# Optimization experiments

Hardware: AMD Instinct MI355X
Metric: run time of the kernel (lower is better)

## Reference

```python
import jax, jax.numpy as jnp
import numpy as np

EPS = 1e-5
NEG_SLOPE = 0.2

def _conv1x1(x, w):
    # x: (B,C,N,K), w: (O,C) -> (B,O,N,K)
    return jnp.einsum('oc,bcnk->bonk', w, x)

def _bn(x, g, b, m, v):
    scale = g / jnp.sqrt(v + EPS)
    return x * scale[None, :, None, None] + (b - m * scale)[None, :, None, None]

def _lrelu(x):
    return jnp.where(x > 0, x, NEG_SLOPE * x)

def setup_inputs() -> dict:
    key = jax.random.key(0)
    specs = {
        'x': ((8, 6, 8192, 20), 'randn'),
        'trans_w': ((64, 6), 'randn'), 'trans_g': ((64,), 'rand'), 'trans_b': ((64,), 'randn'),
        'trans_m': ((64,), 'randn'), 'trans_v': ((64,), 'rand'),
        'pos_w1': ((64, 3), 'randn'), 'pos_g': ((64,), 'rand'), 'pos_b': ((64,), 'randn'),
        'pos_m': ((64,), 'randn'), 'pos_v': ((64,), 'rand'),
        'pos_w2': ((64, 64), 'randn'), 'pos_b2': ((64,), 'randn'),
        'gate_w1': ((16, 6), 'randn'), 'gate_g': ((16,), 'rand'), 'gate_b': ((16,), 'randn'),
        'gate_m': ((16,), 'randn'), 'gate_v': ((16,), 'rand'),
        'gate_w2': ((1, 16), 'randn'), 'gate_b2': ((1,), 'ones'),
        'attn_w1': ((16, 6), 'randn'), 'attn_g': ((16,), 'rand'), 'attn_b': ((16,), 'randn'),
        'attn_m': ((16,), 'randn'), 'attn_v': ((16,), 'rand'),
        'attn_w2': ((64, 16), 'randn'), 'attn_b2': ((64,), 'randn'),
    }
    out = {}
    for i, (name, (shape, fill)) in enumerate(specs.items()):
        k = jax.random.fold_in(key, i)
        if fill == 'randn':
            out[name] = jax.random.normal(k, shape, dtype=jnp.float32) * 0.1
        elif fill == 'rand':
            out[name] = jax.random.uniform(k, shape, dtype=jnp.float32)
        else:  # ones (gate bias init to 2.0 in original; scale ones)
            out[name] = jnp.ones(shape, dtype=jnp.float32) * 2.0
    return out

def reference(x, trans_w, trans_g, trans_b, trans_m, trans_v,
              pos_w1, pos_g, pos_b, pos_m, pos_v, pos_w2, pos_b2,
              gate_w1, gate_g, gate_b, gate_m, gate_v, gate_w2, gate_b2,
              attn_w1, attn_g, attn_b, attn_m, attn_v, attn_w2, attn_b2):
    in_channels = 3
    rel_pos = x[:, in_channels:in_channels + 3, :, :]  # (B,3,N,K)
    # pos_net: conv(3->C) + BN + LReLU + conv(C->C, bias)
    pos_h = _lrelu(_bn(_conv1x1(rel_pos, pos_w1), pos_g, pos_b, pos_m, pos_v))
    pos_enc = _conv1x1(pos_h, pos_w2) + pos_b2[None, :, None, None]
    # trans: conv(2*Cin->C) + BN + LReLU
    trans_feat = _lrelu(_bn(_conv1x1(x, trans_w), trans_g, trans_b, trans_m, trans_v)) + pos_enc
    # gate_net: conv(6->16)+BN+LReLU+conv(16->1,bias)+sigmoid (dropout=0 in eval)
    gate_h = _lrelu(_bn(_conv1x1(x, gate_w1), gate_g, gate_b, gate_m, gate_v))
    gate_map = jax.nn.sigmoid(_conv1x1(gate_h, gate_w2) + gate_b2[None, :, None, None])  # (B,1,N,K)
    clean_feat = trans_feat * gate_map
    # attn_net: conv(6->16)+BN+LReLU+conv(16->C,bias), then + pos_enc, softmax over K
    attn_h = _lrelu(_bn(_conv1x1(x, attn_w1), attn_g, attn_b, attn_m, attn_v))
    attn_logits = _conv1x1(attn_h, attn_w2) + attn_b2[None, :, None, None] + pos_enc
    attn_weights = jax.nn.softmax(attn_logits, axis=-1)
    out_attn = (trans_feat * attn_weights).sum(axis=-1)  # (B,C,N)
    out_max = clean_feat.max(axis=-1)                    # (B,C,N)
    return out_attn + out_max
```

## Files before the change

kernel.cpp:

```cpp
#include <hip/hip_runtime.h>
#include <math.h>

#define NEG 0.2f
#define EPSV 1e-5f

typedef _Float16 v8h __attribute__((ext_vector_type(8)));
typedef _Float16 v4h __attribute__((ext_vector_type(4)));
typedef _Float16 v2h __attribute__((ext_vector_type(2)));
typedef __fp16   f16x2 __attribute__((ext_vector_type(2)));
typedef float    v4f __attribute__((ext_vector_type(4)));

__device__ __forceinline__ float lrelu(float v) { return fmaxf(v, NEG * v); }
__device__ __forceinline__ v4f lrelu4(v4f v) {
    return __builtin_elementwise_max(v, v * NEG);
}
__device__ __forceinline__ v2h lreluh2(v2h v) {
    return __builtin_elementwise_max(v, v * (_Float16)NEG);
}

__device__ __forceinline__ v2h pk(float a, float b) {
    union { f16x2 i; v2h o; } u;
    u.i = __builtin_amdgcn_cvt_pkrtz(a, b);
    return u.o;
}

#define MFMA(a, b, c) __builtin_amdgcn_mfma_f32_16x16x32_f16((a), (b), (c), 0, 0, 0)

__global__ __launch_bounds__(256, 1)
void gsl_mfma(const float* __restrict__ x,
              const float* __restrict__ trans_w, const float* __restrict__ trans_g,
              const float* __restrict__ trans_b, const float* __restrict__ trans_m,
              const float* __restrict__ trans_v,
              const float* __restrict__ pos_w1, const float* __restrict__ pos_g,
              const float* __restrict__ pos_b, const float* __restrict__ pos_m,
              const float* __restrict__ pos_v, const float* __restrict__ pos_w2,
              const float* __restrict__ pos_b2,
              const float* __restrict__ gate_w1, const float* __restrict__ gate_g,
              const float* __restrict__ gate_b, const float* __restrict__ gate_m,
              const float* __restrict__ gate_v, const float* __restrict__ gate_w2,
              const float* __restrict__ gate_b2,
              const float* __restrict__ attn_w1, const float* __restrict__ attn_g,
              const float* __restrict__ attn_b, const float* __restrict__ attn_m,
              const float* __restrict__ attn_v, const float* __restrict__ attn_w2,
              const float* __restrict__ attn_b2,
              float* __restrict__ out)
{
    __shared__ _Float16 WH[3840];
    __shared__ float    PB2[64];
    __shared__ _Float16 PHB[4][2][1152];
    __shared__ _Float16 AHB[4][2][448];

    const int tid  = threadIdx.x;
    const int wv   = tid >> 6;
    const int lane = tid & 63;
    const int p    = lane & 15;
    const int q    = lane >> 4;

    const int b = blockIdx.x >> 7;
    const int n = ((blockIdx.x & 127) << 6) | (wv << 4) | p;

    {
        _Float16* AH0 = &AHB[wv][0][0];
        const v4h zh = {(_Float16)0.f, (_Float16)0.f, (_Float16)0.f, (_Float16)0.f};
        for (int i = lane; i < 224; i += 64) *(v4h*)(AH0 + 4 * i) = zh;
    }

    if (tid < 64) {
        const int c = tid;
        float sp = pos_g[c] * rsqrtf(pos_v[c] + EPSV);
        float bp = pos_b[c] - pos_m[c] * sp;
        _Float16* row = WH + (c >> 4) * 640 + (c & 15) * 40;
        for (int k = 0; k < 40; ++k) {
            float v = (k >= 3 && k < 6) ? pos_w1[c * 3 + (k - 3)] * sp
                                        : ((k == 6) ? bp : 0.f);
            row[k] = (_Float16)v;
        }
        PB2[c] = pos_b2[c];
    } else if (tid < 80) {
        const int j = tid - 64;
        float sa = attn_g[j] * rsqrtf(attn_v[j] + EPSV);
        float ba = attn_b[j] - attn_m[j] * sa;
        _Float16* row = WH + 2560 + j * 40;
        for (int k = 0; k < 40; ++k)
            row[k] = (_Float16)((k < 6) ? attn_w1[j * 6 + k] * sa
                                        : ((k == 6) ? ba : 0.f));
    } else if (tid < 96) {
        const int j = tid - 80;
        float sg = gate_g[j] * rsqrtf(gate_v[j] + EPSV);
        float bg = gate_b[j] - gate_m[j] * sg;
        _Float16* row = WH + 3200 + j * 40;
        for (int k = 0; k < 40; ++k)
            row[k] = (_Float16)((k < 6) ? gate_w1[j * 6 + k] * sg
                                        : ((k == 6) ? bg : 0.f));
    }

    v8h W2f[4][2], WTf[4], WA2f[4];
    #pragma unroll
    for (int mt = 0; mt < 4; ++mt) {
        const int ch = mt * 16 + p;
        #pragma unroll
        for (int h = 0; h < 2; ++h)
            #pragma unroll
            for (int i = 0; i < 8; ++i)
                W2f[mt][h][i] = (_Float16)pos_w2[ch * 64 + h * 32 + q * 8 + i];
        #pragma unroll
        for (int i = 0; i < 8; ++i) {
            int k = q * 8 + i;
            WA2f[mt][i] = (k < 16) ? (_Float16)attn_w2[ch * 16 + k] : (_Float16)0.f;
        }
        float st = trans_g[ch] * rsqrtf(trans_v[ch] + EPSV);
        float bt = trans_b[ch] - trans_m[ch] * st;
        #pragma unroll
        for (int i = 0; i < 8; ++i) {
            int k = q * 8 + i;
            float v = (k < 6) ? trans_w[ch * 6 + k] * st : ((k == 6) ? bt : 0.f);
            WTf[mt][i] = (_Float16)v;
        }
    }
    float g2w[4];
    #pragma unroll
    for (int r = 0; r < 4; ++r) g2w[r] = gate_w2[4 * q + r];
    const float gb2v = gate_b2[0];

    __syncthreads();

    const _Float16* const WP1p = WH + p * 40 + q * 8;
    const _Float16* const WA1p = WH + 2560 + p * 40 + q * 8;
    const _Float16* const WG1p = WH + 3200 + p * 40 + q * 8;
    const float* const    PB2p = PB2 + 4 * q;

    _Float16* const PHbase = &PHB[wv][0][0];
    _Float16* const AHbase = &AHB[wv][0][0];

    const v4f zero = {0.f, 0.f, 0.f, 0.f};
    v4f den[4], num[4], cmx[4];
    #pragma unroll
    for (int mt = 0; mt < 4; ++mt) {
        den[mt] = zero; num[mt] = zero;
        cmx[mt] = (v4f){-3.4e38f, -3.4e38f, -3.4e38f, -3.4e38f};
    }

    const float* xb = x + ((size_t)(b * 6) * 8192 + n) * 20;

    float nx[6];
    #pragma unroll
    for (int c = 0; c < 6; ++c) nx[c] = xb[(size_t)c * 163840];

    v8h xv_cur;
    {
        union { v8h v; v2h h[4]; } u;
        u.h[0] = pk(nx[0], nx[1]);
        u.h[1] = pk(nx[2], nx[3]);
        u.h[2] = pk(nx[4], nx[5]);
        u.h[3] = (v2h){(_Float16)1.f, (_Float16)0.f};
        xv_cur = u.v;
    }
    #pragma unroll
    for (int c = 0; c < 6; ++c) nx[c] = xb[(size_t)c * 163840 + 1];

    {
        v4f php[4];
        #pragma unroll
        for (int mt = 0; mt < 4; ++mt)
            php[mt] = MFMA(*(const v8h*)(WP1p + mt * 640), xv_cur, zero);
        v4f ahp = MFMA(*(const v8h*)WA1p, xv_cur, zero);
        _Float16* PHW = PHbase + p * 72 + 4 * q;
        #pragma unroll
        for (int mt = 0; mt < 4; ++mt) {
            union { v4h v; v2h h[2]; } u;
            u.h[0] = lreluh2(pk(php[mt][0], php[mt][1]));
            u.h[1] = lreluh2(pk(php[mt][2], php[mt][3]));
            *(v4h*)(PHW + mt * 16) = u.v;
        }
        union { v4h v; v2h h[2]; } ua;
        ua.h[0] = lreluh2(pk(ahp[0], ahp[1]));
        ua.h[1] = lreluh2(pk(ahp[2], ahp[3]));
        *(v4h*)(AHbase + p * 24 + 4 * q) = ua.v;
    }

    #pragma unroll 1
    for (int k = 0; k < 20; ++k) {
        const int sel = k & 1;
        _Float16* PH = PHbase + sel * 1152;
        _Float16* AH = AHbase + sel * 448;
        v8h phf0 = *(const v8h*)(PH + p * 72 + 8 * q);
        v8h phf1 = *(const v8h*)(PH + p * 72 + 32 + 8 * q);
        v8h ahf  = *(const v8h*)(AH + p * 24 + 8 * q);

        v8h xv_nxt = xv_cur;
        if (k < 19) {
            union { v8h v; v2h h[4]; } u;
            u.h[0] = pk(nx[0], nx[1]);
            u.h[1] = pk(nx[2], nx[3]);
            u.h[2] = pk(nx[4], nx[5]);
            u.h[3] = (v2h){(_Float16)1.f, (_Float16)0.f};
            xv_nxt = u.v;
            const int kn = (k < 18) ? k + 2 : 19;
            #pragma unroll
            for (int c = 0; c < 6; ++c) nx[c] = xb[(size_t)c * 163840 + kn];

            v4f php[4];
            #pragma unroll
            for (int mt = 0; mt < 4; ++mt)
                php[mt] = MFMA(*(const v8h*)(WP1p + mt * 640), xv_nxt, zero);
            v4f ahp = MFMA(*(const v8h*)WA1p, xv_nxt, zero);
            _Float16* PHW = PHbase + (sel ^ 1) * 1152 + p * 72 + 4 * q;
            #pragma unroll
            for (int mt = 0; mt < 4; ++mt) {
                union { v4h v; v2h h[2]; } uu;
                uu.h[0] = lreluh2(pk(php[mt][0], php[mt][1]));
                uu.h[1] = lreluh2(pk(php[mt][2], php[mt][3]));
                *(v4h*)(PHW + mt * 16) = uu.v;
            }
            union { v4h v; v2h h[2]; } ua;
            ua.h[0] = lreluh2(pk(ahp[0], ahp[1]));
            ua.h[1] = lreluh2(pk(ahp[2], ahp[3]));
            *(v4h*)(AHbase + (sel ^ 1) * 448 + p * 24 + 4 * q) = ua.v;
        }

        v4f tfa[4];
        #pragma unroll
        for (int mt = 0; mt < 4; ++mt) tfa[mt] = MFMA(WTf[mt], xv_cur, zero);
        v4f ghp = MFMA(*(const v8h*)WG1p, xv_cur, zero);
        float ga = 0.f;
        #pragma unroll
        for (int r = 0; r < 4; ++r) ga += g2w[r] * lrelu(ghp[r]);
        ga += __shfl_xor(ga, 16);
        ga += __shfl_xor(ga, 32);
        const float gate = 1.f / (1.f + __expf(-(ga + gb2v)));

        v4f pe[4];
        #pragma unroll
        for (int mt = 0; mt < 4; ++mt) {
            pe[mt] = MFMA(W2f[mt][0], phf0, *(const v4f*)(PB2p + mt * 16));
            pe[mt] = MFMA(W2f[mt][1], phf1, pe[mt]);
        }

        #pragma unroll
        for (int mt = 0; mt < 4; ++mt) {
            v4f tfv = lrelu4(tfa[mt]) + pe[mt];
            pe[mt] = MFMA(WA2f[mt], ahf, pe[mt]);
            v4f e;
            #pragma unroll
            for (int r = 0; r < 4; ++r) e[r] = __expf(pe[mt][r]);
            den[mt] += e;
            num[mt] += tfv * e;
            cmx[mt] = __builtin_elementwise_max(cmx[mt], tfv * gate);
        }
        xv_cur = xv_nxt;
    }

    #pragma unroll
    for (int mt = 0; mt < 4; ++mt) {
        #pragma unroll
        for (int r = 0; r < 4; ++r) {
            const int ch = mt * 16 + 4 * q + r;
            out[((size_t)(b * 64 + ch)) * 8192 + n] =
                num[mt][r] / den[mt][r] + cmx[mt][r];
        }
    }
}

extern "C" void kernel_launch(void* const* d_in, const int* in_sizes, int n_in,
                              void* d_out, int out_size, void* d_ws, size_t ws_size,
                              hipStream_t stream) {
    const float* x       = (const float*)d_in[0];
    const float* trans_w = (const float*)d_in[1];
    const float* trans_g = (const float*)d_in[2];
    const float* trans_b = (const float*)d_in[3];
    const float* trans_m = (const float*)d_in[4];
    const float* trans_v = (const float*)d_in[5];
    const float* pos_w1  = (const float*)d_in[6];
    const float* pos_g   = (const float*)d_in[7];
    const float* pos_b   = (const float*)d_in[8];
    const float* pos_m   = (const float*)d_in[9];
    const float* pos_v   = (const float*)d_in[10];
    const float* pos_w2  = (const float*)d_in[11];
    const float* pos_b2  = (const float*)d_in[12];
    const float* gate_w1 = (const float*)d_in[13];
    const float* gate_g  = (const float*)d_in[14];
    const float* gate_b  = (const float*)d_in[15];
    const float* gate_m  = (const float*)d_in[16];
    const float* gate_v  = (const float*)d_in[17];
    const float* gate_w2 = (const float*)d_in[18];
    const float* gate_b2 = (const float*)d_in[19];
    const float* attn_w1 = (const float*)d_in[20];
    const float* attn_g  = (const float*)d_in[21];
    const float* attn_b  = (const float*)d_in[22];
    const float* attn_m  = (const float*)d_in[23];
    const float* attn_v  = (const float*)d_in[24];
    const float* attn_w2 = (const float*)d_in[25];
    const float* attn_b2 = (const float*)d_in[26];
    float* out = (float*)d_out;

    gsl_mfma<<<1024, 256, 0, stream>>>(
        x, trans_w, trans_g, trans_b, trans_m, trans_v,
        pos_w1, pos_g, pos_b, pos_m, pos_v, pos_w2, pos_b2,
        gate_w1, gate_g, gate_b, gate_m, gate_v, gate_w2, gate_b2,
        attn_w1, attn_g, attn_b, attn_m, attn_v, attn_w2, attn_b2,
        out);
}
```

Before: 197.9 us.

## Stage per-wave x tile into LDS with coalesced float4 loads

Instead of each lane issuing strided scalar global loads of x for every k step, each wave now loads its 16-point x tile once with coalesced float4 reads, converts it to fp16 and stores it transposed into shared memory. The MFMA B operand for each k is then read from LDS as one vector load. The attention-hidden buffer is also shrunk, and its zero-initialisation is dropped by indexing with (q&1)*8. This adds roughly 20KB of LDS per block, which could reduce occupancy, and the transposed scalar LDS stores may hit bank conflicts.

New measurement: 195.7 us. Within noise of the previous version (-1.1%).

```diff
diff --git a/kernel.cpp b/kernel.cpp
--- a/kernel.cpp
+++ b/kernel.cpp
@@ -48,7 +48,8 @@
     __shared__ _Float16 WH[3840];
     __shared__ float    PB2[64];
     __shared__ _Float16 PHB[4][2][1152];
-    __shared__ _Float16 AHB[4][2][448];
+    __shared__ _Float16 AHB[4][2][288];
+    __shared__ _Float16 XSB[4][2560];
 
     const int tid  = threadIdx.x;
     const int wv   = tid >> 6;
@@ -56,13 +57,35 @@
     const int p    = lane & 15;
     const int q    = lane >> 4;
 
-    const int b = blockIdx.x >> 7;
-    const int n = ((blockIdx.x & 127) << 6) | (wv << 4) | p;
+    const int b  = blockIdx.x >> 7;
+    const int n0 = ((blockIdx.x & 127) << 6) | (wv << 4);
+    const int n  = n0 | p;
 
     {
-        _Float16* AH0 = &AHB[wv][0][0];
-        const v4h zh = {(_Float16)0.f, (_Float16)0.f, (_Float16)0.f, (_Float16)0.f};
-        for (int i = lane; i < 224; i += 64) *(v4h*)(AH0 + 4 * i) = zh;
+        const float* xw = x + ((size_t)b * 6 * 8192 + n0) * 20;
+        _Float16* XS = &XSB[wv][0];
+        #pragma unroll
+        for (int i = 0; i < 8; ++i) {
+            int idx = i * 64 + lane;
+            if (idx < 480) {
+                int c  = idx / 80;
+                int rm = idx - c * 80;
+                int pt = rm / 5;
+                int k0 = (rm - pt * 5) * 4;
+                const float4 v = *(const float4*)(xw + (size_t)c * 163840 + pt * 20 + k0);
+                _Float16* dst = XS + pt * 8 + c;
+                dst[(k0 + 0) * 128] = (_Float16)v.x;
+                dst[(k0 + 1) * 128] = (_Float16)v.y;
+                dst[(k0 + 2) * 128] = (_Float16)v.z;
+                dst[(k0 + 3) * 128] = (_Float16)v.w;
+            }
+        }
+        #pragma unroll
+        for (int i = 0; i < 5; ++i) {
+            int idx = i * 64 + lane;
+            int k = idx >> 4, pt = idx & 15;
+            *(v2h*)(XS + k * 128 + pt * 8 + 6) = (v2h){(_Float16)1.f, (_Float16)0.f};
+        }
     }
 
     if (tid < 64) {
@@ -128,9 +151,12 @@
     const _Float16* const WA1p = WH + 2560 + p * 40 + q * 8;
     const _Float16* const WG1p = WH + 3200 + p * 40 + q * 8;
     const float* const    PB2p = PB2 + 4 * q;
+    const _Float16* const XS   = &XSB[wv][0];
 
     _Float16* const PHbase = &PHB[wv][0][0];
     _Float16* const AHbase = &AHB[wv][0][0];
+
+    const int ahq = (q & 1) * 8;
 
     const v4f zero = {0.f, 0.f, 0.f, 0.f};
     v4f den[4], num[4], cmx[4];
@@ -140,24 +166,7 @@
         cmx[mt] = (v4f){-3.4e38f, -3.4e38f, -3.4e38f, -3.4e38f};
     }
 
-    const float* xb = x + ((size_t)(b * 6) * 8192 + n) * 20;
-
-    float nx[6];
-    #pragma unroll
-    for (int c = 0; c < 6; ++c) nx[c] = xb[(size_t)c * 163840];
-
-    v8h xv_cur;
-    {
-        union { v8h v; v2h h[4]; } u;
-        u.h[0] = pk(nx[0], nx[1]);
-        u.h[1] = pk(nx[2], nx[3]);
-        u.h[2] = pk(nx[4], nx[5]);
-        u.h[3] = (v2h){(_Float16)1.f, (_Float16)0.f};
-        xv_cur = u.v;
-    }
-    #pragma unroll
-    for (int c = 0; c < 6; ++c) nx[c] = xb[(size_t)c * 163840 + 1];
-
+    v8h xv_cur = *(const v8h*)(XS + p * 8);
     {
         v4f php[4];
         #pragma unroll
@@ -175,30 +184,21 @@
         union { v4h v; v2h h[2]; } ua;
         ua.h[0] = lreluh2(pk(ahp[0], ahp[1]));
         ua.h[1] = lreluh2(pk(ahp[2], ahp[3]));
-        *(v4h*)(AHbase + p * 24 + 4 * q) = ua.v;
+        *(v4h*)(AHbase + p * 16 + 4 * q) = ua.v;
     }
 
     #pragma unroll 1
     for (int k = 0; k < 20; ++k) {
         const int sel = k & 1;
         _Float16* PH = PHbase + sel * 1152;
-        _Float16* AH = AHbase + sel * 448;
+        _Float16* AH = AHbase + sel * 288;
         v8h phf0 = *(const v8h*)(PH + p * 72 + 8 * q);
         v8h phf1 = *(const v8h*)(PH + p * 72 + 32 + 8 * q);
-        v8h ahf  = *(const v8h*)(AH + p * 24 + 8 * q);
+        v8h ahf  = *(const v8h*)(AH + p * 16 + ahq);
 
         v8h xv_nxt = xv_cur;
         if (k < 19) {
-            union { v8h v; v2h h[4]; } u;
-            u.h[0] = pk(nx[0], nx[1]);
-            u.h[1] = pk(nx[2], nx[3]);
-            u.h[2] = pk(nx[4], nx[5]);
-            u.h[3] = (v2h){(_Float16)1.f, (_Float16)0.f};
-            xv_nxt = u.v;
-            const int kn = (k < 18) ? k + 2 : 19;
-            #pragma unroll
-            for (int c = 0; c < 6; ++c) nx[c] = xb[(size_t)c * 163840 + kn];
-
+            xv_nxt = *(const v8h*)(XS + (k + 1) * 128 + p * 8);
             v4f php[4];
             #pragma unroll
             for (int mt = 0; mt < 4; ++mt)
@@ -215,7 +215,7 @@
             union { v4h v; v2h h[2]; } ua;
             ua.h[0] = lreluh2(pk(ahp[0], ahp[1]));
             ua.h[1] = lreluh2(pk(ahp[2], ahp[3]));
-            *(v4h*)(AHbase + (sel ^ 1) * 448 + p * 24 + 4 * q) = ua.v;
+            *(v4h*)(AHbase + (sel ^ 1) * 288 + p * 16 + 4 * q) = ua.v;
         }
 
         v4f tfa[4];
```
